# Kernel tuning notes

Measured on AMD Instinct MI355X. Metric: run time of the kernel, lower is better.

The kernel has to match this reference:

```python
import jax, jax.numpy as jnp
import numpy as np

EPS = 1e-5

def hardsigmoid(x):
    # torch F.hardsigmoid: clip(x/6 + 0.5, 0, 1)
    return jnp.clip(x / 6.0 + 0.5, 0.0, 1.0)

def setup_inputs() -> dict:
    T, B, D = 2048, 8, 1024
    key = jax.random.key(0)
    k1, k2 = jax.random.split(key)
    x = jax.random.normal(k1, (T, B, D), dtype=jnp.float32)
    c = jnp.zeros((B, D), dtype=jnp.float32)
    # params
    w_ufr = jax.random.normal(k2, (3 * D, D), dtype=jnp.float32) * (1.0 / np.sqrt(D))
    gamma = jnp.ones((D,), dtype=jnp.float32)
    beta = jnp.zeros((D,), dtype=jnp.float32)
    return {"x": x, "c": c, "w_ufr": w_ufr, "gamma": gamma, "beta": beta}

def reference(x, c, w_ufr, gamma, beta):
    residual = x
    # LayerNorm over last dim
    mu = jnp.mean(x, axis=-1, keepdims=True)
    var = jnp.mean(jnp.square(x - mu), axis=-1, keepdims=True)
    x_norm = (x - mu) * jax.lax.rsqrt(var + EPS) * gamma + beta
    # fused projection to u, f, r: (T,B,D) @ (D,3D)
    ufr = jnp.einsum('tbd,ed->tbe', x_norm, w_ufr)
    u, f, r = jnp.split(ufr, 3, axis=-1)
    f_gate = hardsigmoid(f)
    r_gate = hardsigmoid(r)
    # diagonal linear recurrence: c_t = f_t * c_{t-1} + (1 - f_t) * u_t
    def step(c_prev, inputs):
        ft, ut = inputs
        c_curr = ft * c_prev + (1.0 - ft) * ut
        return c_curr, c_curr
    c_last, c_all = jax.lax.scan(step, c, (f_gate, u))
    tanh_approx = c_all / (1.0 + jnp.abs(c_all))  # softsign
    hs = r_gate * tanh_approx + (1.0 - r_gate) * x_norm
    return (residual + hs, c_last)
```

## Files before the change

kernel.cpp:

```cpp
#include <hip/hip_runtime.h>
#include <stdint.h>


#define T_SEQ 2048
#define BATCH 8
#define DIM 1024
#define M_SZ (T_SEQ * BATCH)
#define N_SZ (3 * DIM)
#define K_SZ DIM
#define NCHUNK 32
#define CLEN (T_SEQ / NCHUNK)

#define GBM 256
#define GBN 256
#define GBK 32
#define NKT (K_SZ / GBK)

typedef __attribute__((ext_vector_type(8))) __bf16 bf16x8;
typedef __attribute__((ext_vector_type(4))) float f32x4;

__device__ __forceinline__ unsigned short f2bf(float f) {
  unsigned int u = __float_as_uint(f);
  u += 0x7FFFu + ((u >> 16) & 1u);
  return (unsigned short)(u >> 16);
}
__device__ __forceinline__ float bf2f(unsigned short s) {
  return __uint_as_float(((unsigned int)s) << 16);
}
__device__ __forceinline__ void gload16(const void* g, void* l) {
  __builtin_amdgcn_global_load_lds(
      (__attribute__((address_space(1))) void*)const_cast<void*>(g),
      (__attribute__((address_space(3))) void*)l, 16, 0, 0);
}

__global__ __launch_bounds__(256) void cvt_kernel(const float* __restrict__ w,
                                                  unsigned short* __restrict__ wb) {
  const int i = blockIdx.x * 256 + threadIdx.x;
  const float4 v = reinterpret_cast<const float4*>(w)[i];
  ushort4 o;
  o.x = f2bf(v.x); o.y = f2bf(v.y); o.z = f2bf(v.z); o.w = f2bf(v.w);
  reinterpret_cast<ushort4*>(wb)[i] = o;
}

__global__ __launch_bounds__(256) void ln_kernel(const float* __restrict__ x,
                                                 const float* __restrict__ gamma,
                                                 const float* __restrict__ beta,
                                                 unsigned short* __restrict__ xn) {
  const int row = blockIdx.x;
  const int tid = threadIdx.x;
  const float4 v = reinterpret_cast<const float4*>(x + (size_t)row * DIM)[tid];
  float s = v.x + v.y + v.z + v.w;
  float q = v.x * v.x + v.y * v.y + v.z * v.z + v.w * v.w;
#pragma unroll
  for (int off = 32; off > 0; off >>= 1) {
    s += __shfl_down(s, off);
    q += __shfl_down(q, off);
  }
  __shared__ float sbuf[8];
  const int wv = tid >> 6, ln = tid & 63;
  if (ln == 0) { sbuf[wv] = s; sbuf[4 + wv] = q; }
  __syncthreads();
  s = sbuf[0] + sbuf[1] + sbuf[2] + sbuf[3];
  q = sbuf[4] + sbuf[5] + sbuf[6] + sbuf[7];
  const float mu = s * (1.0f / DIM);
  const float rstd = rsqrtf(q * (1.0f / DIM) - mu * mu + 1e-5f);
  const float4 g = reinterpret_cast<const float4*>(gamma)[tid];
  const float4 b = reinterpret_cast<const float4*>(beta)[tid];
  ushort4 o;
  o.x = f2bf((v.x - mu) * rstd * g.x + b.x);
  o.y = f2bf((v.y - mu) * rstd * g.y + b.y);
  o.z = f2bf((v.z - mu) * rstd * g.z + b.z);
  o.w = f2bf((v.w - mu) * rstd * g.w + b.w);
  reinterpret_cast<ushort4*>(xn + (size_t)row * DIM)[tid] = o;
}

__global__ __launch_bounds__(512) void gemm_kernel(const unsigned short* __restrict__ A,
                                                   const unsigned short* __restrict__ W,
                                                   unsigned short* __restrict__ C) {
  __shared__ unsigned short smem[2 * 4 * GBM * GBK];
  const int tid = threadIdx.x;
  const int lane = tid & 63;
  const int wid = tid >> 6;
  const int wm = wid >> 2, wn = wid & 3;
  const int bm0 = blockIdx.y * GBM, bn0 = blockIdx.x * GBN;

  const int stgRow = wid * 32 + (lane >> 2);
  const int stgCol = ((lane & 3) ^ ((lane >> 3) & 3)) * 8;
  const unsigned short* gA = A + (size_t)(bm0 + stgRow) * K_SZ + stgCol;
  const unsigned short* gB = W + (size_t)(bn0 + stgRow) * K_SZ + stgCol;
  unsigned short* sAb = smem + wid * 32 * GBK;
  unsigned short* sBb = smem + 4 * GBM * GBK + wid * 32 * GBK;

#define STAGE(bufi, t) do {                                        \
    const size_t ko_ = (size_t)(t) * GBK;                          \
    unsigned short* sa_ = sAb + (bufi) * (GBM * GBK);              \
    unsigned short* sb_ = sBb + (bufi) * (GBN * GBK);              \
    gload16(gA + ko_, sa_);                                        \
    gload16(gA + ko_ + (size_t)16 * K_SZ, sa_ + 16 * GBK);         \
    gload16(gB + ko_, sb_);                                        \
    gload16(gB + ko_ + (size_t)16 * K_SZ, sb_ + 16 * GBK);         \
  } while (0)

  f32x4 acc[8][4] = {};
  const int fr = lane & 15;
  const int ko8 = ((lane >> 4) ^ ((fr >> 1) & 3)) * 8;

  STAGE(0, 0);
  STAGE(1, 1);
  STAGE(2, 2);
  asm volatile("s_waitcnt vmcnt(8)" ::: "memory");
  __builtin_amdgcn_s_barrier();
  asm volatile("" ::: "memory");

  for (int kt = 0; kt < NKT; ++kt) {
    const int cur = kt & 3;
    if (kt < NKT - 3) STAGE((kt + 3) & 3, kt + 3);

    const unsigned short* sa = smem + cur * (GBM * GBK);
    const unsigned short* sb = smem + 4 * GBM * GBK + cur * (GBN * GBK);
    bf16x8 af[8], bf[4];
#pragma unroll
    for (int i = 0; i < 8; i++)
      af[i] = *(const bf16x8*)&sa[(wm * 128 + i * 16 + fr) * GBK + ko8];
#pragma unroll
    for (int j = 0; j < 4; j++)
      bf[j] = *(const bf16x8*)&sb[(wn * 64 + j * 16 + fr) * GBK + ko8];

    __builtin_amdgcn_s_setprio(1);
#pragma unroll
    for (int i = 0; i < 8; i++)
#pragma unroll
      for (int j = 0; j < 4; j++)
        acc[i][j] = __builtin_amdgcn_mfma_f32_16x16x32_bf16(af[i], bf[j], acc[i][j], 0, 0, 0);
    __builtin_amdgcn_s_setprio(0);

    if (kt < NKT - 3)       asm volatile("s_waitcnt vmcnt(8)" ::: "memory");
    else if (kt == NKT - 3) asm volatile("s_waitcnt vmcnt(4)" ::: "memory");
    else if (kt == NKT - 2) asm volatile("s_waitcnt vmcnt(0)" ::: "memory");
    if (kt < NKT - 1) {
      __builtin_amdgcn_s_barrier();
      asm volatile("" ::: "memory");
    }
  }
#undef STAGE

  const int gate = (bn0 >= DIM);
  const int fq = lane >> 4;
#pragma unroll
  for (int i = 0; i < 8; i++) {
#pragma unroll
    for (int j = 0; j < 4; j++) {
      const int col = bn0 + wn * 64 + j * 16 + fr;
      size_t base = (size_t)(bm0 + wm * 128 + i * 16 + fq * 4) * N_SZ + col;
#pragma unroll
      for (int r = 0; r < 4; r++) {
        float v = acc[i][j][r];
        if (gate) v = fminf(fmaxf(v * (1.0f / 6.0f) + 0.5f, 0.0f), 1.0f);
        C[base + (size_t)r * N_SZ] = f2bf(v);
      }
    }
  }
}

__global__ __launch_bounds__(256) void scan1_kernel(const unsigned short* __restrict__ ufr,
                                                    float* __restrict__ Ac,
                                                    float* __restrict__ Bc) {
  const int lin = blockIdx.x * 256 + threadIdx.x;
  const int d = lin & (DIM - 1);
  const int b = (lin >> 10) & (BATCH - 1);
  const int g = lin >> 13;
  const unsigned short* p = ufr + (size_t)(g * CLEN) * (BATCH * N_SZ) + (size_t)b * N_SZ + d;
  float Aa = 1.0f, Bb = 0.0f;
#pragma unroll 8
  for (int t = 0; t < CLEN; t++) {
    const float u = bf2f(p[0]);
    const float f = bf2f(p[DIM]);
    Aa *= f;
    Bb = f * Bb + (1.0f - f) * u;
    p += BATCH * N_SZ;
  }
  Ac[lin] = Aa;
  Bc[lin] = Bb;
}

__global__ __launch_bounds__(256) void scan2_kernel(const float* __restrict__ Ac,
                                                    const float* __restrict__ Bc,
                                                    const float* __restrict__ c0,
                                                    float* __restrict__ cstart,
                                                    float* __restrict__ clast) {
  const int lin = blockIdx.x * 256 + threadIdx.x;
  float c = c0[lin];
#pragma unroll
  for (int g = 0; g < NCHUNK; g++) {
    cstart[g * (BATCH * DIM) + lin] = c;
    c = Ac[g * (BATCH * DIM) + lin] * c + Bc[g * (BATCH * DIM) + lin];
  }
  clast[lin] = c;
}

__global__ __launch_bounds__(256) void scan3_kernel(const unsigned short* __restrict__ ufr,
                                                    const unsigned short* __restrict__ xn,
                                                    const float* __restrict__ x,
                                                    const float* __restrict__ cstart,
                                                    float* __restrict__ out) {
  const int lin = blockIdx.x * 256 + threadIdx.x;
  const int d = lin & (DIM - 1);
  const int b = (lin >> 10) & (BATCH - 1);
  const int g = lin >> 13;
  float c = cstart[g * (BATCH * DIM) + b * DIM + d];
  const unsigned short* p = ufr + (size_t)(g * CLEN) * (BATCH * N_SZ) + (size_t)b * N_SZ + d;
  size_t xo = (size_t)(g * CLEN) * (BATCH * DIM) + (size_t)b * DIM + d;
#pragma unroll 4
  for (int t = 0; t < CLEN; t++) {
    const float u = bf2f(p[0]);
    const float f = bf2f(p[DIM]);
    const float r = bf2f(p[2 * DIM]);
    c = f * c + (1.0f - f) * u;
    const float ts = c / (1.0f + fabsf(c));
    const float xv = bf2f(xn[xo]);
    out[xo] = x[xo] + r * ts + (1.0f - r) * xv;
    p += BATCH * N_SZ;
    xo += BATCH * DIM;
  }
}

extern "C" void kernel_launch(void* const* d_in, const int* in_sizes, int n_in,
                              void* d_out, int out_size, void* d_ws, size_t ws_size,
                              hipStream_t stream) {
  const float* x = (const float*)d_in[0];
  const float* c0 = (const float*)d_in[1];
  const float* w = (const float*)d_in[2];
  const float* gamma = (const float*)d_in[3];
  const float* beta = (const float*)d_in[4];
  float* out = (float*)d_out;
  float* clast = out + (size_t)M_SZ * DIM;

  char* ws = (char*)d_ws;
  unsigned short* xn = (unsigned short*)ws;
  unsigned short* ufr = (unsigned short*)(ws + 33554432ull);
  float* Ac = (float*)(ws + 134217728ull);
  float* Bc = (float*)(ws + 135266304ull);
  float* cst = (float*)(ws + 136314880ull);
  unsigned short* wb = (unsigned short*)(ws + 137363456ull);

  cvt_kernel<<<(N_SZ * K_SZ / 4) / 256, 256, 0, stream>>>(w, wb);
  ln_kernel<<<M_SZ, 256, 0, stream>>>(x, gamma, beta, xn);
  dim3 ggrid(N_SZ / GBN, M_SZ / GBM);
  gemm_kernel<<<ggrid, 512, 0, stream>>>(xn, wb, ufr);
  scan1_kernel<<<(NCHUNK * BATCH * DIM) / 256, 256, 0, stream>>>(ufr, Ac, Bc);
  scan2_kernel<<<(BATCH * DIM) / 256, 256, 0, stream>>>(Ac, Bc, c0, cst, clast);
  scan3_kernel<<<(NCHUNK * BATCH * DIM) / 256, 256, 0, stream>>>(ufr, xn, x, cst, out);
}
```

Measured before the change: 206.8 us.

## Load GEMM B operand directly into registers and remap workgroups across XCDs

The GEMM now skips LDS staging for the weight (B) tile and loads each wave's B fragments straight from global memory into registers, double-buffered two k-steps ahead. This halves LDS use and removes the B LDS reads. The launch grid becomes 1-D and block indices are remapped so consecutive tiles land on the same XCD, which is meant to improve L2 reuse. The cost is redundant global B loads across waves that share columns, plus more VGPR pressure from the register double buffer.

```diff
diff --git a/kernel.cpp b/kernel.cpp
--- a/kernel.cpp
+++ b/kernel.cpp
@@ -15,6 +15,8 @@
 #define GBN 256
 #define GBK 32
 #define NKT (K_SZ / GBK)
+#define NBX (N_SZ / GBN)
+#define NWG (NBX * (M_SZ / GBM))
 
 typedef __attribute__((ext_vector_type(8))) __bf16 bf16x8;
 typedef __attribute__((ext_vector_type(4))) float f32x4;
@@ -77,72 +79,107 @@
 __global__ __launch_bounds__(512) void gemm_kernel(const unsigned short* __restrict__ A,
                                                    const unsigned short* __restrict__ W,
                                                    unsigned short* __restrict__ C) {
-  __shared__ unsigned short smem[2 * 4 * GBM * GBK];
+  __shared__ unsigned short smem[4 * GBM * GBK];
   const int tid = threadIdx.x;
   const int lane = tid & 63;
   const int wid = tid >> 6;
   const int wm = wid >> 2, wn = wid & 3;
-  const int bm0 = blockIdx.y * GBM, bn0 = blockIdx.x * GBN;
-
-  const int stgRow = wid * 32 + (lane >> 2);
+
+  const int wg = (blockIdx.x & 7) * (NWG / 8) + (blockIdx.x >> 3);
+  const int bn0 = (wg % NBX) * GBN;
+  const int bm0 = (wg / NBX) * GBM;
+
+  const int stgRow = wid * 16 + (lane >> 2);
   const int stgCol = ((lane & 3) ^ ((lane >> 3) & 3)) * 8;
-  const unsigned short* gA = A + (size_t)(bm0 + stgRow) * K_SZ + stgCol;
-  const unsigned short* gB = W + (size_t)(bn0 + stgRow) * K_SZ + stgCol;
-  unsigned short* sAb = smem + wid * 32 * GBK;
-  unsigned short* sBb = smem + 4 * GBM * GBK + wid * 32 * GBK;
-
-#define STAGE(bufi, t) do {                                        \
+  const unsigned short* gA0 = A + (size_t)(bm0 + stgRow) * K_SZ + stgCol;
+  const unsigned short* gA1 = gA0 + (size_t)128 * K_SZ;
+  unsigned short* sA0 = smem + (wid * 16) * GBK;
+  unsigned short* sA1 = smem + (128 + wid * 16) * GBK;
+
+#define STAGE_A(bufi, t) do {                                      \
     const size_t ko_ = (size_t)(t) * GBK;                          \
-    unsigned short* sa_ = sAb + (bufi) * (GBM * GBK);              \
-    unsigned short* sb_ = sBb + (bufi) * (GBN * GBK);              \
-    gload16(gA + ko_, sa_);                                        \
-    gload16(gA + ko_ + (size_t)16 * K_SZ, sa_ + 16 * GBK);         \
-    gload16(gB + ko_, sb_);                                        \
-    gload16(gB + ko_ + (size_t)16 * K_SZ, sb_ + 16 * GBK);         \
+    gload16(gA0 + ko_, sA0 + (bufi) * (GBM * GBK));                \
+    gload16(gA1 + ko_, sA1 + (bufi) * (GBM * GBK));                \
   } while (0)
 
-  f32x4 acc[8][4] = {};
   const int fr = lane & 15;
   const int ko8 = ((lane >> 4) ^ ((fr >> 1) & 3)) * 8;
 
-  STAGE(0, 0);
-  STAGE(1, 1);
-  STAGE(2, 2);
-  asm volatile("s_waitcnt vmcnt(8)" ::: "memory");
+  unsigned int bvo[4];
+#pragma unroll
+  for (int j = 0; j < 4; j++)
+    bvo[j] = (unsigned int)(bn0 + wn * 64 + j * 16 + fr) * (K_SZ * 2) + (lane >> 4) * 16;
+
+  bf16x8 b0[4], b1[4];
+#define BLOAD(breg, t) do {                                        \
+    const unsigned int to_ = (unsigned int)(t) * (GBK * 2);        \
+    asm volatile("global_load_dwordx4 %0, %1, %2"                  \
+        : "=v"(breg[0]) : "v"(bvo[0] + to_), "s"(W));              \
+    asm volatile("global_load_dwordx4 %0, %1, %2"                  \
+        : "=v"(breg[1]) : "v"(bvo[1] + to_), "s"(W));              \
+    asm volatile("global_load_dwordx4 %0, %1, %2"                  \
+        : "=v"(breg[2]) : "v"(bvo[2] + to_), "s"(W));              \
+    asm volatile("global_load_dwordx4 %0, %1, %2"                  \
+        : "=v"(breg[3]) : "v"(bvo[3] + to_), "s"(W));              \
+  } while (0)
+
+  f32x4 acc[8][4] = {};
+
+  STAGE_A(0, 0);
+  STAGE_A(1, 1);
+  STAGE_A(2, 2);
+  BLOAD(b0, 0);
+  BLOAD(b1, 1);
+  asm volatile("s_waitcnt vmcnt(4)" ::: "memory");
+  __builtin_amdgcn_sched_barrier(0);
   __builtin_amdgcn_s_barrier();
   asm volatile("" ::: "memory");
 
-  for (int kt = 0; kt < NKT; ++kt) {
-    const int cur = kt & 3;
-    if (kt < NKT - 3) STAGE((kt + 3) & 3, kt + 3);
-
-    const unsigned short* sa = smem + cur * (GBM * GBK);
-    const unsigned short* sb = smem + 4 * GBM * GBK + cur * (GBN * GBK);
-    bf16x8 af[8], bf[4];
+#define BODY(kt, breg, VM) do {                                              \
+    const int cur_ = (kt) & 3;                                               \
+    if ((kt) <= NKT - 4) STAGE_A(((kt) + 3) & 3, (kt) + 3);                  \
+    const unsigned short* sa_ = smem + cur_ * (GBM * GBK);                   \
+    bf16x8 af_[8];                                                           \
+    _Pragma("unroll")                                                        \
+    for (int i = 0; i < 8; i++)                                              \
+      af_[i] = *(const bf16x8*)&sa_[(wm * 128 + i * 16 + fr) * GBK + ko8];   \
+    __builtin_amdgcn_s_setprio(1);                                           \
+    _Pragma("unroll")                                                        \
+    for (int i = 0; i < 8; i++)                                              \
+      _Pragma("unroll")                                                      \
+      for (int j = 0; j < 4; j++)                                            \
+        acc[i][j] = __builtin_amdgcn_mfma_f32_16x16x32_bf16(af_[i], breg[j], \
+                                                            acc[i][j], 0, 0, 0); \
+    __builtin_amdgcn_s_setprio(0);                                           \
+    if ((kt) <= NKT - 3) BLOAD(breg, (kt) + 2);                              \
+    asm volatile("s_waitcnt vmcnt(" #VM ")" ::: "memory");                   \
+    __builtin_amdgcn_sched_barrier(0);                                       \
+    __builtin_amdgcn_s_barrier();                                            \
+    asm volatile("" ::: "memory");                                           \
+  } while (0)
+
+  for (int kt = 0; kt < NKT - 4; kt += 2) {
+    BODY(kt, b0, 6);
+    BODY(kt + 1, b1, 6);
+  }
+  BODY(NKT - 4, b0, 6);
+  BODY(NKT - 3, b1, 4);
+  BODY(NKT - 2, b0, 0);
+  {
+    const unsigned short* sa_ = smem + ((NKT - 1) & 3) * (GBM * GBK);
+    bf16x8 af_[8];
 #pragma unroll
     for (int i = 0; i < 8; i++)
-      af[i] = *(const bf16x8*)&sa[(wm * 128 + i * 16 + fr) * GBK + ko8];
-#pragma unroll
-    for (int j = 0; j < 4; j++)
-      bf[j] = *(const bf16x8*)&sb[(wn * 64 + j * 16 + fr) * GBK + ko8];
-
-    __builtin_amdgcn_s_setprio(1);
+      af_[i] = *(const bf16x8*)&sa_[(wm * 128 + i * 16 + fr) * GBK + ko8];
 #pragma unroll
     for (int i = 0; i < 8; i++)
 #pragma unroll
       for (int j = 0; j < 4; j++)
-        acc[i][j] = __builtin_amdgcn_mfma_f32_16x16x32_bf16(af[i], bf[j], acc[i][j], 0, 0, 0);
-    __builtin_amdgcn_s_setprio(0);
-
-    if (kt < NKT - 3)       asm volatile("s_waitcnt vmcnt(8)" ::: "memory");
-    else if (kt == NKT - 3) asm volatile("s_waitcnt vmcnt(4)" ::: "memory");
-    else if (kt == NKT - 2) asm volatile("s_waitcnt vmcnt(0)" ::: "memory");
-    if (kt < NKT - 1) {
-      __builtin_amdgcn_s_barrier();
-      asm volatile("" ::: "memory");
-    }
-  }
-#undef STAGE
+        acc[i][j] = __builtin_amdgcn_mfma_f32_16x16x32_bf16(af_[i], b1[j], acc[i][j], 0, 0, 0);
+  }
+#undef BODY
+#undef BLOAD
+#undef STAGE_A
 
   const int gate = (bn0 >= DIM);
   const int fq = lane >> 4;
@@ -245,8 +282,7 @@
 
   cvt_kernel<<<(N_SZ * K_SZ / 4) / 256, 256, 0, stream>>>(w, wb);
   ln_kernel<<<M_SZ, 256, 0, stream>>>(x, gamma, beta, xn);
-  dim3 ggrid(N_SZ / GBN, M_SZ / GBM);
-  gemm_kernel<<<ggrid, 512, 0, stream>>>(xn, wb, ufr);
+  gemm_kernel<<<NWG, 512, 0, stream>>>(xn, wb, ufr);
   scan1_kernel<<<(NCHUNK * BATCH * DIM) / 256, 256, 0, stream>>>(ufr, Ac, Bc);
   scan2_kernel<<<(BATCH * DIM) / 256, 256, 0, stream>>>(Ac, Bc, c0, cst, clast);
   scan3_kernel<<<(NCHUNK * BATCH * DIM) / 256, 256, 0, stream>>>(ufr, xn, x, cst, out);
```

Measured after the change: 225.1 us. +8.9%, slower.
